# Kernel tuning notes

Hardware: AMD Instinct MI355X
Metric: run time of the kernel (lower is better)

The kernel has to match this reference:

```python
import jax, jax.numpy as jnp
import numpy as np

B, N, H = 2, 4096, 2048
NH, HD = 16, 128
BLK = 256
EPS = 1e-6


def setup_inputs() -> dict:
    key = jax.random.key(0)
    ks = jax.random.split(key, 5)
    scale = 0.02
    x = jax.random.normal(ks[0], (B, N, H), dtype=jnp.float32)
    # ALiBi-style per-head slopes, shape [h,1,1]
    slopes = (1.0 / (2.0 ** (8.0 * np.arange(1, NH + 1) / NH))).astype(np.float32)
    slope_rate = jnp.asarray(slopes).reshape(NH, 1, 1)
    w_qkv = jax.random.normal(ks[1], (3 * NH * HD, H), dtype=jnp.float32) * scale
    w_gate = jax.random.normal(ks[2], (NH * HD, H), dtype=jnp.float32) * scale
    w_out = jax.random.normal(ks[3], (H, NH * HD), dtype=jnp.float32) * scale
    norm_w = jnp.ones((NH * HD,), dtype=jnp.float32)
    return {"hidden_states": x, "slope_rate": slope_rate, "w_qkv": w_qkv,
            "w_gate": w_gate, "w_out": w_out, "norm_w": norm_w}


def _lightning_attn(x, slope_rate, w_qkv, w_gate, w_out, norm_w):
    b, n, _ = x.shape
    h, d = NH, HD
    nb = n // BLK
    # qkv projection + activation
    qkv = jax.nn.silu(jnp.einsum('bnf,of->bno', x, w_qkv))        # [b,n,3hd]
    qkv = qkv.reshape(b, n, h, 3 * d)
    q, k, v = jnp.split(qkv, 3, axis=-1)                          # each [b,n,h,d]
    q = q.transpose(0, 2, 1, 3)                                   # [b,h,n,d]
    k = k.transpose(0, 2, 1, 3)
    v = v.transpose(0, 2, 1, 3)

    s = slope_rate.astype(jnp.float32)                            # [h,1,1]
    arr = jnp.arange(1, BLK + 1, dtype=jnp.float32)               # 1..BLOCK
    q_decay = jnp.exp(-s * arr[:, None])                          # [h,BLK,1]
    k_decay = jnp.exp(-s * (BLK - arr)[:, None])                  # [h,BLK,1]
    idx = arr[:, None] - arr[None, :]                             # [BLK,BLK]
    diag_decay = jnp.where(idx >= 0, jnp.exp(-s * idx), 0.0)      # [h,BLK,BLK]
    block_decay = jnp.exp(-s * BLK)                               # [h,1,1]

    # split sequence into blocks; scan axis leading
    qb = q.reshape(b, h, nb, BLK, d).transpose(2, 0, 1, 3, 4)     # [nb,b,h,BLK,d]
    kb = k.reshape(b, h, nb, BLK, d).transpose(2, 0, 1, 3, 4)
    vb = v.reshape(b, h, nb, BLK, d).transpose(2, 0, 1, 3, 4)

    def step(kv, blk):
        qi, ki, vi = blk                                          # [b,h,BLK,d]
        o_inter = jnp.einsum('bhmd,bhde->bhme', qi * q_decay, kv)
        qk = jnp.einsum('bhmd,bhnd->bhmn', qi, ki) * diag_decay
        o_intra = jnp.einsum('bhmn,bhne->bhme', qk, vi)
        kv_new = block_decay * kv + jnp.einsum('bhmd,bhme->bhde', ki * k_decay, vi)
        return kv_new, o_inter + o_intra

    kv0 = jnp.zeros((b, h, d, d), dtype=jnp.float32)
    _, out = jax.lax.scan(step, kv0, (qb, kb, vb))                # [nb,b,h,BLK,d]
    out = out.transpose(1, 2, 0, 3, 4).reshape(b, h, n, d)        # [b,h,n,d]
    out = out.transpose(0, 2, 1, 3).reshape(b, n, h * d)          # [b,n,h*d]

    # RMSNorm (fp32)
    var = jnp.mean(out * out, axis=-1, keepdims=True)
    out = norm_w * (out * jax.lax.rsqrt(var + EPS))

    gate = jax.nn.sigmoid(jnp.einsum('bnf,of->bno', x, w_gate))
    return jnp.einsum('bno,fo->bnf', gate * out, w_out)


def reference(hidden_states, slope_rate, w_qkv, w_gate, w_out, norm_w):
    return _lightning_attn(hidden_states, slope_rate, w_qkv, w_gate, w_out, norm_w)
```

## Files before the change

kernel.cpp:

```cpp
#include <hip/hip_runtime.h>
#include <hip/hip_bf16.h>
#include <stdint.h>


typedef __bf16 bf16_t;
typedef __bf16 bf16x8 __attribute__((ext_vector_type(8)));
typedef __bf16 bf16x4 __attribute__((ext_vector_type(4)));
typedef float  f32x4  __attribute__((ext_vector_type(4)));

#define AS1C(p) ((const __attribute__((address_space(1))) void*)(p))
#define AS3(p)  ((__attribute__((address_space(3))) void*)(p))

__global__ __launch_bounds__(256) void cvt_kernel(const float* __restrict__ s,
                                                  bf16_t* __restrict__ d, int n4) {
    int i = blockIdx.x * blockDim.x + threadIdx.x;
    const int stride = gridDim.x * blockDim.x;
    for (; i < n4; i += stride) {
        float4 v = ((const float4*)s)[i];
        bf16x4 o;
        o[0] = (bf16_t)v.x; o[1] = (bf16_t)v.y; o[2] = (bf16_t)v.z; o[3] = (bf16_t)v.w;
        ((bf16x4*)d)[i] = o;
    }
}

template <int EPI>
__global__ __launch_bounds__(512)
void gemm6(const bf16_t* __restrict__ A, const bf16_t* __restrict__ Bm,
           int M, int N, int K,
           float* __restrict__ outf, bf16_t* __restrict__ outb,
           bf16_t* __restrict__ qb, bf16_t* __restrict__ kb, bf16_t* __restrict__ vb,
           const float* __restrict__ slopes) {
    __shared__ char lds[2][65536];
    const int tid = threadIdx.x, w = tid >> 6, lane = tid & 63;
    const int l15 = lane & 15, lq = lane >> 4;
    const int wr = w >> 2, wc = w & 3;

    const int nwg = gridDim.x;
    const int cpx = nwg >> 3;
    const int id = blockIdx.x;
    const int sw = (id & 7) * cpx + (id >> 3);
    const int gx = N >> 8;
    const int tm = (sw / gx) << 8;
    const int tn = (sw % gx) << 8;
    const int nt = K >> 6;

    auto stageA1 = [&](char* dst, int t1, int j) {
        const bf16_t* base = A + (size_t)tm * K + t1 * 64;
        const int c = tid + j * 512;
        const int r = c >> 3, sl = c & 7;
        __builtin_amdgcn_global_load_lds(
            AS1C(base + (size_t)r * K + ((sl ^ (r & 7)) << 3)),
            AS3(dst + c * 16), 16, 0, 0);
    };
    auto stageB1 = [&](char* dst, int t1, int j) {
        const bf16_t* base = Bm + (size_t)tn * K + t1 * 64;
        const int c = tid + j * 512;
        const int r = c >> 3, sl = c & 7;
        __builtin_amdgcn_global_load_lds(
            AS1C(base + (size_t)r * K + ((sl ^ (r & 7)) << 3)),
            AS3(dst + 32768 + c * 16), 16, 0, 0);
    };

    f32x4 acc[8][4] = {};

    {
        char* d0 = &lds[0][0];
        stageA1(d0, 0, 0); stageA1(d0, 0, 2);
        stageB1(d0, 0, 0); stageB1(d0, 0, 1); stageB1(d0, 0, 2); stageB1(d0, 0, 3);
        stageA1(d0, 0, 1); stageA1(d0, 0, 3);
    }

    for (int t = 0; t < nt; ++t) {
        const char* cur = &lds[t & 1][0];
        char* nxt = &lds[1 - (t & 1)][0];
        const bool pre = (t + 1 < nt);

        asm volatile("s_waitcnt vmcnt(2)" ::: "memory");
        __builtin_amdgcn_s_barrier();
        __builtin_amdgcn_sched_barrier(0);
        bf16x8 bfr[4][2], af[4][2];
#pragma unroll
        for (int n = 0; n < 4; ++n)
#pragma unroll
            for (int kk = 0; kk < 2; ++kk) {
                const int row = wc * 64 + n * 16 + l15;
                bfr[n][kk] = *(const bf16x8*)(cur + 32768 + row * 128 + ((((kk << 2) | lq) ^ (row & 7)) << 4));
            }
#pragma unroll
        for (int m = 0; m < 4; ++m)
#pragma unroll
            for (int kk = 0; kk < 2; ++kk) {
                const int row = wr * 128 + m * 16 + l15;
                af[m][kk] = *(const bf16x8*)(cur + row * 128 + ((((kk << 2) | lq) ^ (row & 7)) << 4));
            }
        if (pre) {
            stageA1(nxt, t + 1, 0); stageA1(nxt, t + 1, 2);
            stageB1(nxt, t + 1, 0); stageB1(nxt, t + 1, 1);
            stageB1(nxt, t + 1, 2); stageB1(nxt, t + 1, 3);
        }
        __builtin_amdgcn_s_setprio(1);
#pragma unroll
        for (int m = 0; m < 4; ++m)
#pragma unroll
            for (int n = 0; n < 4; ++n)
#pragma unroll
                for (int kk = 0; kk < 2; ++kk)
                    acc[m][n] = __builtin_amdgcn_mfma_f32_16x16x32_bf16(af[m][kk], bfr[n][kk], acc[m][n], 0, 0, 0);
        __builtin_amdgcn_s_setprio(0);

        if (pre) asm volatile("s_waitcnt vmcnt(6)" ::: "memory");
        else     asm volatile("s_waitcnt vmcnt(0)" ::: "memory");
        __builtin_amdgcn_s_barrier();
        __builtin_amdgcn_sched_barrier(0);
#pragma unroll
        for (int m = 0; m < 4; ++m)
#pragma unroll
            for (int kk = 0; kk < 2; ++kk) {
                const int row = wr * 128 + 64 + m * 16 + l15;
                af[m][kk] = *(const bf16x8*)(cur + row * 128 + ((((kk << 2) | lq) ^ (row & 7)) << 4));
            }
        if (pre) {
            stageA1(nxt, t + 1, 1); stageA1(nxt, t + 1, 3);
        }
        __builtin_amdgcn_s_setprio(1);
#pragma unroll
        for (int m = 0; m < 4; ++m)
#pragma unroll
            for (int n = 0; n < 4; ++n)
#pragma unroll
                for (int kk = 0; kk < 2; ++kk)
                    acc[4 + m][n] = __builtin_amdgcn_mfma_f32_16x16x32_bf16(af[m][kk], bfr[n][kk], acc[4 + m][n], 0, 0, 0);
        __builtin_amdgcn_s_setprio(0);
    }

#pragma unroll
    for (int m = 0; m < 8; ++m) {
#pragma unroll
        for (int n = 0; n < 4; ++n) {
            const int colb = tn + wc * 64 + n * 16;
            if (EPI == 2) {
#pragma unroll
                for (int r = 0; r < 4; ++r) {
                    const int row = tm + wr * 128 + m * 16 + lq * 4 + r;
                    outf[(size_t)row * N + colb + l15] = acc[m][n][r];
                }
            } else if (EPI == 1) {
#pragma unroll
                for (int r = 0; r < 4; ++r) {
                    const int row = tm + wr * 128 + m * 16 + lq * 4 + r;
                    const float v = acc[m][n][r];
                    outb[(size_t)row * N + colb + l15] = (bf16_t)(1.f / (1.f + __expf(-v)));
                }
            } else {
                const int head = colb / 384;
                const int jj = colb % 384;
#pragma unroll
                for (int r = 0; r < 4; ++r) {
                    const int row = tm + wr * 128 + m * 16 + lq * 4 + r;
                    const int bidx = row >> 12;
                    const int nn = row & 4095;
                    const float v = acc[m][n][r];
                    const float sv = v / (1.f + __expf(-v));
                    const size_t base = ((size_t)(bidx * 16 + head) * 4096 + nn) * 128;
                    if (jj < 128)       qb[base + jj + l15]       = (bf16_t)sv;
                    else if (jj < 256)  kb[base + jj - 128 + l15] = (bf16_t)sv;
                    else                vb[base + jj - 256 + l15] = (bf16_t)sv;
                }
            }
        }
    }
}

__global__ __launch_bounds__(256)
void transpose_128(const bf16_t* __restrict__ src, bf16_t* __restrict__ dst) {
    __shared__ bf16_t t[64][72];
    const int bh = blockIdx.z;
    const int n0 = blockIdx.x * 64, d0 = blockIdx.y * 64;
    const int tid = threadIdx.x;
    const int r = tid >> 2, cg = (tid & 3) * 16;
    const bf16_t* sp = src + ((size_t)bh * 4096 + n0 + r) * 128 + d0 + cg;
    *(bf16x8*)&t[r][cg] = *(const bf16x8*)sp;
    *(bf16x8*)&t[r][cg + 8] = *(const bf16x8*)(sp + 8);
    __syncthreads();
    bf16_t* dp = dst + ((size_t)bh * 128 + d0 + r) * 4096 + n0 + cg;
#pragma unroll
    for (int i = 0; i < 16; ++i) dp[i] = t[cg + i][r];
}

__global__ __launch_bounds__(256)
void pass_ct(const bf16_t* __restrict__ vT, const bf16_t* __restrict__ kT,
             float* __restrict__ CT, const float* __restrict__ slopes) {
    const int idx = blockIdx.x, bh = idx >> 4, j = idx & 15;
    const float s = slopes[bh & 15];
    const int tid = threadIdx.x, w = tid >> 6, lane = tid & 63;
    const int l15 = lane & 15, lq = lane >> 4;
    const int we = (w & 1) * 64, wd = (w >> 1) * 64;
    const bf16_t* va = vT + (size_t)bh * 524288 + j * 256;
    const bf16_t* ka = kT + (size_t)bh * 524288 + j * 256;
    f32x4 acc[4][4] = {};
#pragma unroll
    for (int kk = 0; kk < 8; ++kk) {
        float fdec[8];
#pragma unroll
        for (int t = 0; t < 8; ++t)
            fdec[t] = __expf(-s * (float)(255 - (kk * 32 + lq * 8 + t)));
        bf16x8 af[4], bfv[4];
#pragma unroll
        for (int et = 0; et < 4; ++et)
            af[et] = *(const bf16x8*)(va + (size_t)(we + et * 16 + l15) * 4096 + kk * 32 + lq * 8);
#pragma unroll
        for (int dt = 0; dt < 4; ++dt) {
            bf16x8 raw = *(const bf16x8*)(ka + (size_t)(wd + dt * 16 + l15) * 4096 + kk * 32 + lq * 8);
#pragma unroll
            for (int t = 0; t < 8; ++t) bfv[dt][t] = (bf16_t)((float)raw[t] * fdec[t]);
        }
#pragma unroll
        for (int et = 0; et < 4; ++et)
#pragma unroll
            for (int dt = 0; dt < 4; ++dt)
                acc[et][dt] = __builtin_amdgcn_mfma_f32_16x16x32_bf16(af[et], bfv[dt], acc[et][dt], 0, 0, 0);
    }
    float* out = CT + (size_t)idx * 16384;
#pragma unroll
    for (int et = 0; et < 4; ++et)
#pragma unroll
        for (int dt = 0; dt < 4; ++dt)
#pragma unroll
            for (int r = 0; r < 4; ++r)
                out[(size_t)(we + et * 16 + lq * 4 + r) * 128 + wd + dt * 16 + l15] = acc[et][dt][r];
}

__global__ __launch_bounds__(256)
void scan_kv(const float* __restrict__ CT, bf16_t* __restrict__ states,
             const float* __restrict__ slopes) {
    const int bh = blockIdx.x;
    const float s = slopes[bh & 15];
    const float bd = __expf(-s * 256.f);
    const int tid = threadIdx.x;
    const int e = tid >> 1, d0 = (tid & 1) * 64;
    const size_t off = (size_t)e * 128 + d0;
    float kv[64];
#pragma unroll
    for (int i = 0; i < 64; ++i) kv[i] = 0.f;
    for (int j = 0; j < 16; ++j) {
        const size_t blk = (size_t)(bh * 16 + j) * 16384;
        bf16_t* st = states + blk + off;
#pragma unroll
        for (int i = 0; i < 64; ++i) st[i] = (bf16_t)kv[i];
        const float* c = CT + blk + off;
#pragma unroll
        for (int i = 0; i < 64; ++i) kv[i] = bd * kv[i] + c[i];
    }
}

__global__ __launch_bounds__(512)
void pass_attn(const bf16_t* __restrict__ qb, const bf16_t* __restrict__ kb,
               const bf16_t* __restrict__ vT, const bf16_t* __restrict__ states,
               const float* __restrict__ slopes, float* __restrict__ outattn) {
    __shared__ bf16_t scratch[8][32][48];
    const int idx = blockIdx.x, bh = idx >> 4, j = idx & 15;
    const int b = bh >> 4, h = bh & 15;
    const int tid = threadIdx.x, w = tid >> 6, lane = tid & 63;
    const int l15 = lane & 15, lq = lane >> 4;
    const float s = slopes[h];
    f32x4 o[2][8] = {};
    float rowf[8];
#pragma unroll
    for (int mt = 0; mt < 2; ++mt)
#pragma unroll
        for (int r = 0; r < 4; ++r) rowf[mt * 4 + r] = __expf(-s * (float)(mt * 16 + lq * 4 + r));

    const size_t qrow = (size_t)bh * 4096 + j * 256;
    const bf16_t* qbp = qb + (qrow + w * 32) * 128;
    const bf16_t* kbp = kb + qrow * 128;
    const bf16_t* vtp = vT + (size_t)bh * 524288 + (size_t)j * 256;

    for (int nc = 0; nc <= w; ++nc) {
        f32x4 sacc[2][2] = {};
#pragma unroll
        for (int kq = 0; kq < 4; ++kq) {
            bf16x8 a2[2], b2[2];
#pragma unroll
            for (int mt = 0; mt < 2; ++mt)
                a2[mt] = *(const bf16x8*)(qbp + (size_t)(mt * 16 + l15) * 128 + kq * 32 + lq * 8);
#pragma unroll
            for (int nt = 0; nt < 2; ++nt)
                b2[nt] = *(const bf16x8*)(kbp + (size_t)(nc * 32 + nt * 16 + l15) * 128 + kq * 32 + lq * 8);
#pragma unroll
            for (int mt = 0; mt < 2; ++mt)
#pragma unroll
                for (int nt = 0; nt < 2; ++nt)
                    sacc[mt][nt] = __builtin_amdgcn_mfma_f32_16x16x32_bf16(a2[mt], b2[nt], sacc[mt][nt], 0, 0, 0);
        }
        float colf[2];
#pragma unroll
        for (int nt = 0; nt < 2; ++nt)
            colf[nt] = __expf(s * (float)(nc * 32 + nt * 16 + l15 - w * 32));
#pragma unroll
        for (int mt = 0; mt < 2; ++mt)
#pragma unroll
            for (int nt = 0; nt < 2; ++nt)
#pragma unroll
                for (int r = 0; r < 4; ++r) {
                    const int mloc = mt * 16 + lq * 4 + r;
                    const int nglob = nc * 32 + nt * 16 + l15;
                    const float f = (w * 32 + mloc >= nglob) ? rowf[mt * 4 + r] * colf[nt] : 0.f;
                    scratch[w][mloc][nt * 16 + l15] = (bf16_t)(sacc[mt][nt][r] * f);
                }
        bf16x8 sa[2];
#pragma unroll
        for (int mt = 0; mt < 2; ++mt)
            sa[mt] = *(const bf16x8*)&scratch[w][mt * 16 + l15][lq * 8];
#pragma unroll
        for (int et = 0; et < 8; ++et) {
            bf16x8 bv = *(const bf16x8*)(vtp + (size_t)(et * 16 + l15) * 4096 + nc * 32 + lq * 8);
#pragma unroll
            for (int mt = 0; mt < 2; ++mt)
                o[mt][et] = __builtin_amdgcn_mfma_f32_16x16x32_bf16(sa[mt], bv, o[mt][et], 0, 0, 0);
        }
    }

    float rq[2];
#pragma unroll
    for (int mt = 0; mt < 2; ++mt)
        rq[mt] = __expf(-s * (float)(w * 32 + mt * 16 + l15 + 1));
    const bf16_t* st = states + (size_t)idx * 16384;
#pragma unroll
    for (int kq = 0; kq < 4; ++kq) {
        bf16x8 aq[2];
#pragma unroll
        for (int mt = 0; mt < 2; ++mt) {
            bf16x8 raw = *(const bf16x8*)(qbp + (size_t)(mt * 16 + l15) * 128 + kq * 32 + lq * 8);
#pragma unroll
            for (int t = 0; t < 8; ++t) aq[mt][t] = (bf16_t)((float)raw[t] * rq[mt]);
        }
#pragma unroll
        for (int et = 0; et < 8; ++et) {
            bf16x8 bs = *(const bf16x8*)(st + (size_t)(et * 16 + l15) * 128 + kq * 32 + lq * 8);
#pragma unroll
            for (int mt = 0; mt < 2; ++mt)
                o[mt][et] = __builtin_amdgcn_mfma_f32_16x16x32_bf16(aq[mt], bs, o[mt][et], 0, 0, 0);
        }
    }

    float* op = outattn + ((size_t)b * 4096 + j * 256 + w * 32) * 2048 + h * 128;
#pragma unroll
    for (int mt = 0; mt < 2; ++mt)
#pragma unroll
        for (int et = 0; et < 8; ++et)
#pragma unroll
            for (int r = 0; r < 4; ++r)
                op[(size_t)(mt * 16 + lq * 4 + r) * 2048 + et * 16 + l15] = o[mt][et][r];
}

__global__ __launch_bounds__(256)
void rmsnorm_gate(const float* __restrict__ attn, const bf16_t* __restrict__ gate_s,
                  const float* __restrict__ norm_w, bf16_t* __restrict__ gout) {
    const int row = blockIdx.x, tid = threadIdx.x;
    const float* ap = attn + (size_t)row * 2048 + tid * 8;
    float4 v0 = *(const float4*)(ap);
    float4 v1 = *(const float4*)(ap + 4);
    float av[8] = {v0.x, v0.y, v0.z, v0.w, v1.x, v1.y, v1.z, v1.w};
    float ss = 0.f;
#pragma unroll
    for (int i = 0; i < 8; ++i) ss += av[i] * av[i];
#pragma unroll
    for (int off = 32; off; off >>= 1) ss += __shfl_xor(ss, off);
    __shared__ float red[4];
    if ((tid & 63) == 0) red[tid >> 6] = ss;
    __syncthreads();
    const float rr = rsqrtf((red[0] + red[1] + red[2] + red[3]) * (1.0f / 2048.f) + 1e-6f);
    const bf16x8 g = *(const bf16x8*)(gate_s + (size_t)row * 2048 + tid * 8);
    const float* nw = norm_w + tid * 8;
    bf16x8 res;
#pragma unroll
    for (int i = 0; i < 8; ++i) res[i] = (bf16_t)((float)g[i] * nw[i] * av[i] * rr);
    *(bf16x8*)(gout + (size_t)row * 2048 + tid * 8) = res;
}

extern "C" void kernel_launch(void* const* d_in, const int* in_sizes, int n_in,
                              void* d_out, int out_size, void* d_ws, size_t ws_size,
                              hipStream_t stream) {
    (void)in_sizes; (void)n_in; (void)out_size;
    const float* x      = (const float*)d_in[0];
    const float* slopes = (const float*)d_in[1];
    const float* w_qkv  = (const float*)d_in[2];
    const float* w_gate = (const float*)d_in[3];
    const float* w_out  = (const float*)d_in[4];
    const float* norm_w = (const float*)d_in[5];
    float* out = (float*)d_out;
    char* ws = (char*)d_ws;

    size_t off = 0;
    auto alloc = [&](size_t bytes) { char* p = ws + off; off += (bytes + 255) & ~(size_t)255; return p; };
    bf16_t* xb     = (bf16_t*)alloc(8192ull * 2048 * 2);
    bf16_t* wqkvb  = (bf16_t*)alloc(6144ull * 2048 * 2);
    bf16_t* wgateb = (bf16_t*)alloc(2048ull * 2048 * 2);
    bf16_t* woutb  = (bf16_t*)alloc(2048ull * 2048 * 2);
    bf16_t* qb     = (bf16_t*)alloc(33554432);
    bf16_t* kb     = (bf16_t*)alloc(33554432);
    bf16_t* vb     = (bf16_t*)alloc(33554432);
    bf16_t* vT     = (bf16_t*)alloc(33554432);
    bf16_t* kT     = (bf16_t*)alloc(33554432);
    if (ws_size < off) return;
    float*  CT     = (float*)vb;
    bf16_t* gate_s = kT;
    bf16_t* states = (bf16_t*)wqkvb;
    bf16_t* gout   = qb;

    cvt_kernel<<<2048, 256, 0, stream>>>(x,      xb,     8192 * 2048 / 4);
    cvt_kernel<<<2048, 256, 0, stream>>>(w_qkv,  wqkvb,  6144 * 2048 / 4);
    cvt_kernel<<<1024, 256, 0, stream>>>(w_gate, wgateb, 2048 * 2048 / 4);
    cvt_kernel<<<1024, 256, 0, stream>>>(w_out,  woutb,  2048 * 2048 / 4);
    gemm6<0><<<768, 512, 0, stream>>>(xb, wqkvb, 8192, 6144, 2048,
        nullptr, nullptr, qb, kb, vb, slopes);
    transpose_128<<<dim3(64, 2, 32), 256, 0, stream>>>(vb, vT);
    transpose_128<<<dim3(64, 2, 32), 256, 0, stream>>>(kb, kT);
    pass_ct<<<512, 256, 0, stream>>>(vT, kT, CT, slopes);
    gemm6<1><<<256, 512, 0, stream>>>(xb, wgateb, 8192, 2048, 2048,
        nullptr, gate_s, nullptr, nullptr, nullptr, nullptr);
    scan_kv<<<32, 256, 0, stream>>>(CT, states, slopes);
    pass_attn<<<512, 512, 0, stream>>>(qb, kb, vT, states, slopes, out);
    rmsnorm_gate<<<8192, 256, 0, stream>>>(out, gate_s, norm_w, gout);
    gemm6<2><<<256, 512, 0, stream>>>(gout, woutb, 8192, 2048, 2048,
        out, nullptr, nullptr, nullptr, nullptr, nullptr);
}
```

Baseline: 574.8 us.

## Split GEMM main loop into four phases interleaving LDS reads, prefetch and MFMA

Restructures the bf16 GEMM inner loop from two phases into four smaller phases, each over one k-half and one m-half. Each phase reads a smaller set of A/B fragments from LDS, issues a slice of the next tile's global-to-LDS prefetch, then runs 16 MFMAs. Staging is spread more evenly across phases with adjusted vmcnt waits. The goal is finer overlap of memory traffic and compute and lower register pressure, at the cost of more barriers per iteration.

Result: slower. 591.5 us (+2.9%).

```diff
diff --git a/kernel.cpp b/kernel.cpp
--- a/kernel.cpp
+++ b/kernel.cpp
@@ -69,68 +69,104 @@
         stageB1(d0, 0, 0); stageB1(d0, 0, 1); stageB1(d0, 0, 2); stageB1(d0, 0, 3);
         stageA1(d0, 0, 1); stageA1(d0, 0, 3);
     }
+    asm volatile("s_waitcnt vmcnt(2)" ::: "memory");
+    __builtin_amdgcn_s_barrier();
+    __builtin_amdgcn_sched_barrier(0);
 
     for (int t = 0; t < nt; ++t) {
         const char* cur = &lds[t & 1][0];
         char* nxt = &lds[1 - (t & 1)][0];
         const bool pre = (t + 1 < nt);
-
-        asm volatile("s_waitcnt vmcnt(2)" ::: "memory");
-        __builtin_amdgcn_s_barrier();
-        __builtin_amdgcn_sched_barrier(0);
-        bf16x8 bfr[4][2], af[4][2];
-#pragma unroll
-        for (int n = 0; n < 4; ++n)
-#pragma unroll
-            for (int kk = 0; kk < 2; ++kk) {
-                const int row = wc * 64 + n * 16 + l15;
-                bfr[n][kk] = *(const bf16x8*)(cur + 32768 + row * 128 + ((((kk << 2) | lq) ^ (row & 7)) << 4));
-            }
+        bf16x8 bfr[4][2], af[4];
+
+#pragma unroll
+        for (int n = 0; n < 4; ++n) {
+            const int row = wc * 64 + n * 16 + l15;
+            bfr[n][0] = *(const bf16x8*)(cur + 32768 + row * 128 + ((lq ^ (row & 7)) << 4));
+        }
+#pragma unroll
+        for (int m = 0; m < 4; ++m) {
+            const int row = wr * 128 + m * 16 + l15;
+            af[m] = *(const bf16x8*)(cur + row * 128 + ((lq ^ (row & 7)) << 4));
+        }
+        if (pre) { stageA1(nxt, t + 1, 0); stageA1(nxt, t + 1, 2); }
+        __builtin_amdgcn_s_barrier();
+        asm volatile("s_waitcnt lgkmcnt(0)" ::: "memory");
+        __builtin_amdgcn_sched_barrier(0);
+        __builtin_amdgcn_s_setprio(1);
 #pragma unroll
         for (int m = 0; m < 4; ++m)
 #pragma unroll
-            for (int kk = 0; kk < 2; ++kk) {
-                const int row = wr * 128 + m * 16 + l15;
-                af[m][kk] = *(const bf16x8*)(cur + row * 128 + ((((kk << 2) | lq) ^ (row & 7)) << 4));
-            }
-        if (pre) {
-            stageA1(nxt, t + 1, 0); stageA1(nxt, t + 1, 2);
-            stageB1(nxt, t + 1, 0); stageB1(nxt, t + 1, 1);
-            stageB1(nxt, t + 1, 2); stageB1(nxt, t + 1, 3);
-        }
+            for (int n = 0; n < 4; ++n)
+                acc[m][n] = __builtin_amdgcn_mfma_f32_16x16x32_bf16(af[m], bfr[n][0], acc[m][n], 0, 0, 0);
+        __builtin_amdgcn_s_setprio(0);
+        __builtin_amdgcn_s_barrier();
+        __builtin_amdgcn_sched_barrier(0);
+
+#pragma unroll
+        for (int n = 0; n < 4; ++n) {
+            const int row = wc * 64 + n * 16 + l15;
+            bfr[n][1] = *(const bf16x8*)(cur + 32768 + row * 128 + (((4 | lq) ^ (row & 7)) << 4));
+        }
+#pragma unroll
+        for (int m = 0; m < 4; ++m) {
+            const int row = wr * 128 + m * 16 + l15;
+            af[m] = *(const bf16x8*)(cur + row * 128 + (((4 | lq) ^ (row & 7)) << 4));
+        }
+        if (pre) { stageB1(nxt, t + 1, 0); stageB1(nxt, t + 1, 1); }
+        __builtin_amdgcn_s_barrier();
+        asm volatile("s_waitcnt lgkmcnt(0)" ::: "memory");
+        __builtin_amdgcn_sched_barrier(0);
         __builtin_amdgcn_s_setprio(1);
 #pragma unroll
         for (int m = 0; m < 4; ++m)
 #pragma unroll
             for (int n = 0; n < 4; ++n)
-#pragma unroll
-                for (int kk = 0; kk < 2; ++kk)
-                    acc[m][n] = __builtin_amdgcn_mfma_f32_16x16x32_bf16(af[m][kk], bfr[n][kk], acc[m][n], 0, 0, 0);
+                acc[m][n] = __builtin_amdgcn_mfma_f32_16x16x32_bf16(af[m], bfr[n][1], acc[m][n], 0, 0, 0);
         __builtin_amdgcn_s_setprio(0);
-
-        if (pre) asm volatile("s_waitcnt vmcnt(6)" ::: "memory");
+        if (pre) asm volatile("s_waitcnt vmcnt(4)" ::: "memory");
         else     asm volatile("s_waitcnt vmcnt(0)" ::: "memory");
         __builtin_amdgcn_s_barrier();
         __builtin_amdgcn_sched_barrier(0);
+
+#pragma unroll
+        for (int m = 0; m < 4; ++m) {
+            const int row = wr * 128 + 64 + m * 16 + l15;
+            af[m] = *(const bf16x8*)(cur + row * 128 + ((lq ^ (row & 7)) << 4));
+        }
+        if (pre) { stageB1(nxt, t + 1, 2); stageB1(nxt, t + 1, 3); }
+        __builtin_amdgcn_s_barrier();
+        asm volatile("s_waitcnt lgkmcnt(0)" ::: "memory");
+        __builtin_amdgcn_sched_barrier(0);
+        __builtin_amdgcn_s_setprio(1);
 #pragma unroll
         for (int m = 0; m < 4; ++m)
 #pragma unroll
-            for (int kk = 0; kk < 2; ++kk) {
-                const int row = wr * 128 + 64 + m * 16 + l15;
-                af[m][kk] = *(const bf16x8*)(cur + row * 128 + ((((kk << 2) | lq) ^ (row & 7)) << 4));
-            }
-        if (pre) {
-            stageA1(nxt, t + 1, 1); stageA1(nxt, t + 1, 3);
-        }
+            for (int n = 0; n < 4; ++n)
+                acc[4 + m][n] = __builtin_amdgcn_mfma_f32_16x16x32_bf16(af[m], bfr[n][0], acc[4 + m][n], 0, 0, 0);
+        __builtin_amdgcn_s_setprio(0);
+        __builtin_amdgcn_s_barrier();
+        __builtin_amdgcn_sched_barrier(0);
+
+#pragma unroll
+        for (int m = 0; m < 4; ++m) {
+            const int row = wr * 128 + 64 + m * 16 + l15;
+            af[m] = *(const bf16x8*)(cur + row * 128 + (((4 | lq) ^ (row & 7)) << 4));
+        }
+        if (pre) { stageA1(nxt, t + 1, 1); stageA1(nxt, t + 1, 3); }
+        __builtin_amdgcn_s_barrier();
+        asm volatile("s_waitcnt lgkmcnt(0)" ::: "memory");
+        __builtin_amdgcn_sched_barrier(0);
         __builtin_amdgcn_s_setprio(1);
 #pragma unroll
         for (int m = 0; m < 4; ++m)
 #pragma unroll
             for (int n = 0; n < 4; ++n)
-#pragma unroll
-                for (int kk = 0; kk < 2; ++kk)
-                    acc[4 + m][n] = __builtin_amdgcn_mfma_f32_16x16x32_bf16(af[m][kk], bfr[n][kk], acc[4 + m][n], 0, 0, 0);
+                acc[4 + m][n] = __builtin_amdgcn_mfma_f32_16x16x32_bf16(af[m], bfr[n][1], acc[4 + m][n], 0, 0, 0);
         __builtin_amdgcn_s_setprio(0);
+        if (pre) asm volatile("s_waitcnt vmcnt(2)" ::: "memory");
+        __builtin_amdgcn_s_barrier();
+        __builtin_amdgcn_sched_barrier(0);
     }
 
 #pragma unroll
```

## Parallelize kv scan per element, balance causal attention rows, reorder GEMM prefetch

Applied to the files above, without the earlier changes.

The kv-state scan now runs one thread per state element across 2048 blocks instead of 32 blocks each holding 64 registers per thread, so it uses far more of the GPU and its memory accesses are coalesced. In the intra-block attention, each wave now takes two 16-row groups (w and 15-w) instead of one contiguous 32-row group. This evens out the triangular causal work across the waves. The GEMM loop issues its next-tile global prefetches before the LDS fragment reads to start memory traffic earlier. Using smaller 16-row tiles means more K loads and less reuse per MFMA.

New measurement: 551.4 us. -4.1%, faster.

```diff
diff --git a/kernel.cpp b/kernel.cpp
--- a/kernel.cpp
+++ b/kernel.cpp
@@ -78,26 +78,26 @@
         asm volatile("s_waitcnt vmcnt(2)" ::: "memory");
         __builtin_amdgcn_s_barrier();
         __builtin_amdgcn_sched_barrier(0);
-        bf16x8 bfr[4][2], af[4][2];
-#pragma unroll
-        for (int n = 0; n < 4; ++n)
-#pragma unroll
-            for (int kk = 0; kk < 2; ++kk) {
-                const int row = wc * 64 + n * 16 + l15;
-                bfr[n][kk] = *(const bf16x8*)(cur + 32768 + row * 128 + ((((kk << 2) | lq) ^ (row & 7)) << 4));
-            }
-#pragma unroll
-        for (int m = 0; m < 4; ++m)
-#pragma unroll
-            for (int kk = 0; kk < 2; ++kk) {
-                const int row = wr * 128 + m * 16 + l15;
-                af[m][kk] = *(const bf16x8*)(cur + row * 128 + ((((kk << 2) | lq) ^ (row & 7)) << 4));
-            }
         if (pre) {
             stageA1(nxt, t + 1, 0); stageA1(nxt, t + 1, 2);
             stageB1(nxt, t + 1, 0); stageB1(nxt, t + 1, 1);
             stageB1(nxt, t + 1, 2); stageB1(nxt, t + 1, 3);
         }
+        bf16x8 bfr[4][2], af[4][2];
+#pragma unroll
+        for (int n = 0; n < 4; ++n)
+#pragma unroll
+            for (int kk = 0; kk < 2; ++kk) {
+                const int row = wc * 64 + n * 16 + l15;
+                bfr[n][kk] = *(const bf16x8*)(cur + 32768 + row * 128 + ((((kk << 2) | lq) ^ (row & 7)) << 4));
+            }
+#pragma unroll
+        for (int m = 0; m < 4; ++m)
+#pragma unroll
+            for (int kk = 0; kk < 2; ++kk) {
+                const int row = wr * 128 + m * 16 + l15;
+                af[m][kk] = *(const bf16x8*)(cur + row * 128 + ((((kk << 2) | lq) ^ (row & 7)) << 4));
+            }
         __builtin_amdgcn_s_setprio(1);
 #pragma unroll
         for (int m = 0; m < 4; ++m)
@@ -112,6 +112,9 @@
         else     asm volatile("s_waitcnt vmcnt(0)" ::: "memory");
         __builtin_amdgcn_s_barrier();
         __builtin_amdgcn_sched_barrier(0);
+        if (pre) {
+            stageA1(nxt, t + 1, 1); stageA1(nxt, t + 1, 3);
+        }
 #pragma unroll
         for (int m = 0; m < 4; ++m)
 #pragma unroll
@@ -119,9 +122,6 @@
                 const int row = wr * 128 + 64 + m * 16 + l15;
                 af[m][kk] = *(const bf16x8*)(cur + row * 128 + ((((kk << 2) | lq) ^ (row & 7)) << 4));
             }
-        if (pre) {
-            stageA1(nxt, t + 1, 1); stageA1(nxt, t + 1, 3);
-        }
         __builtin_amdgcn_s_setprio(1);
 #pragma unroll
         for (int m = 0; m < 4; ++m)
@@ -233,23 +233,17 @@
 __global__ __launch_bounds__(256)
 void scan_kv(const float* __restrict__ CT, bf16_t* __restrict__ states,
              const float* __restrict__ slopes) {
-    const int bh = blockIdx.x;
+    const int gid = blockIdx.x * 256 + threadIdx.x;
+    const int bh = gid >> 14, elem = gid & 16383;
     const float s = slopes[bh & 15];
     const float bd = __expf(-s * 256.f);
-    const int tid = threadIdx.x;
-    const int e = tid >> 1, d0 = (tid & 1) * 64;
-    const size_t off = (size_t)e * 128 + d0;
-    float kv[64];
-#pragma unroll
-    for (int i = 0; i < 64; ++i) kv[i] = 0.f;
+    const float* c = CT + (size_t)bh * 16 * 16384 + elem;
+    bf16_t* st = states + (size_t)bh * 16 * 16384 + elem;
+    float kv = 0.f;
+#pragma unroll
     for (int j = 0; j < 16; ++j) {
-        const size_t blk = (size_t)(bh * 16 + j) * 16384;
-        bf16_t* st = states + blk + off;
-#pragma unroll
-        for (int i = 0; i < 64; ++i) st[i] = (bf16_t)kv[i];
-        const float* c = CT + blk + off;
-#pragma unroll
-        for (int i = 0; i < 64; ++i) kv[i] = bd * kv[i] + c[i];
+        st[(size_t)j * 16384] = (bf16_t)kv;
+        kv = bd * kv + c[(size_t)j * 16384];
     }
 }
 
@@ -257,100 +251,89 @@
 void pass_attn(const bf16_t* __restrict__ qb, const bf16_t* __restrict__ kb,
                const bf16_t* __restrict__ vT, const bf16_t* __restrict__ states,
                const float* __restrict__ slopes, float* __restrict__ outattn) {
-    __shared__ bf16_t scratch[8][32][48];
+    __shared__ bf16_t scratch[8][16][40];
     const int idx = blockIdx.x, bh = idx >> 4, j = idx & 15;
     const int b = bh >> 4, h = bh & 15;
     const int tid = threadIdx.x, w = tid >> 6, lane = tid & 63;
     const int l15 = lane & 15, lq = lane >> 4;
     const float s = slopes[h];
     f32x4 o[2][8] = {};
-    float rowf[8];
-#pragma unroll
-    for (int mt = 0; mt < 2; ++mt)
-#pragma unroll
-        for (int r = 0; r < 4; ++r) rowf[mt * 4 + r] = __expf(-s * (float)(mt * 16 + lq * 4 + r));
+    float rowf[4];
+#pragma unroll
+    for (int r = 0; r < 4; ++r) rowf[r] = __expf(-s * (float)(lq * 4 + r));
 
     const size_t qrow = (size_t)bh * 4096 + j * 256;
-    const bf16_t* qbp = qb + (qrow + w * 32) * 128;
+    const bf16_t* qbase = qb + qrow * 128;
     const bf16_t* kbp = kb + qrow * 128;
     const bf16_t* vtp = vT + (size_t)bh * 524288 + (size_t)j * 256;
 
-    for (int nc = 0; nc <= w; ++nc) {
-        f32x4 sacc[2][2] = {};
-#pragma unroll
-        for (int kq = 0; kq < 4; ++kq) {
-            bf16x8 a2[2], b2[2];
-#pragma unroll
-            for (int mt = 0; mt < 2; ++mt)
-                a2[mt] = *(const bf16x8*)(qbp + (size_t)(mt * 16 + l15) * 128 + kq * 32 + lq * 8);
-#pragma unroll
-            for (int nt = 0; nt < 2; ++nt)
-                b2[nt] = *(const bf16x8*)(kbp + (size_t)(nc * 32 + nt * 16 + l15) * 128 + kq * 32 + lq * 8);
-#pragma unroll
-            for (int mt = 0; mt < 2; ++mt)
-#pragma unroll
-                for (int nt = 0; nt < 2; ++nt)
-                    sacc[mt][nt] = __builtin_amdgcn_mfma_f32_16x16x32_bf16(a2[mt], b2[nt], sacc[mt][nt], 0, 0, 0);
-        }
-        float colf[2];
-#pragma unroll
-        for (int nt = 0; nt < 2; ++nt)
-            colf[nt] = __expf(s * (float)(nc * 32 + nt * 16 + l15 - w * 32));
-#pragma unroll
-        for (int mt = 0; mt < 2; ++mt)
-#pragma unroll
-            for (int nt = 0; nt < 2; ++nt)
+#pragma unroll
+    for (int gi = 0; gi < 2; ++gi) {
+        const int gg = gi ? (15 - w) : w;
+        const bf16_t* qg = qbase + (size_t)(gg * 16) * 128;
+        const int ncmax = gg >> 1;
+        for (int nc = 0; nc <= ncmax; ++nc) {
+            f32x4 sacc[2] = {};
+#pragma unroll
+            for (int kq = 0; kq < 4; ++kq) {
+                bf16x8 a = *(const bf16x8*)(qg + (size_t)l15 * 128 + kq * 32 + lq * 8);
+                bf16x8 b0 = *(const bf16x8*)(kbp + (size_t)(nc * 32 + l15) * 128 + kq * 32 + lq * 8);
+                bf16x8 b1 = *(const bf16x8*)(kbp + (size_t)(nc * 32 + 16 + l15) * 128 + kq * 32 + lq * 8);
+                sacc[0] = __builtin_amdgcn_mfma_f32_16x16x32_bf16(a, b0, sacc[0], 0, 0, 0);
+                sacc[1] = __builtin_amdgcn_mfma_f32_16x16x32_bf16(a, b1, sacc[1], 0, 0, 0);
+            }
+#pragma unroll
+            for (int nt = 0; nt < 2; ++nt) {
+                const float colf = __expf(s * (float)(nc * 32 + nt * 16 + l15 - gg * 16));
 #pragma unroll
                 for (int r = 0; r < 4; ++r) {
-                    const int mloc = mt * 16 + lq * 4 + r;
+                    const int mloc = lq * 4 + r;
                     const int nglob = nc * 32 + nt * 16 + l15;
-                    const float f = (w * 32 + mloc >= nglob) ? rowf[mt * 4 + r] * colf[nt] : 0.f;
-                    scratch[w][mloc][nt * 16 + l15] = (bf16_t)(sacc[mt][nt][r] * f);
+                    const float f = (gg * 16 + mloc >= nglob) ? rowf[r] * colf : 0.f;
+                    scratch[w][mloc][nt * 16 + l15] = (bf16_t)(sacc[nt][r] * f);
                 }
-        bf16x8 sa[2];
-#pragma unroll
-        for (int mt = 0; mt < 2; ++mt)
-            sa[mt] = *(const bf16x8*)&scratch[w][mt * 16 + l15][lq * 8];
-#pragma unroll
-        for (int et = 0; et < 8; ++et) {
-            bf16x8 bv = *(const bf16x8*)(vtp + (size_t)(et * 16 + l15) * 4096 + nc * 32 + lq * 8);
-#pragma unroll
-            for (int mt = 0; mt < 2; ++mt)
-                o[mt][et] = __builtin_amdgcn_mfma_f32_16x16x32_bf16(sa[mt], bv, o[mt][et], 0, 0, 0);
+            }
+            bf16x8 sa = *(const bf16x8*)&scratch[w][l15][lq * 8];
+#pragma unroll
+            for (int et = 0; et < 8; ++et) {
+                bf16x8 bv = *(const bf16x8*)(vtp + (size_t)(et * 16 + l15) * 4096 + nc * 32 + lq * 8);
+                o[gi][et] = __builtin_amdgcn_mfma_f32_16x16x32_bf16(sa, bv, o[gi][et], 0, 0, 0);
+            }
         }
     }
 
     float rq[2];
-#pragma unroll
-    for (int mt = 0; mt < 2; ++mt)
-        rq[mt] = __expf(-s * (float)(w * 32 + mt * 16 + l15 + 1));
+    rq[0] = __expf(-s * (float)(w * 16 + l15 + 1));
+    rq[1] = __expf(-s * (float)((15 - w) * 16 + l15 + 1));
     const bf16_t* st = states + (size_t)idx * 16384;
 #pragma unroll
     for (int kq = 0; kq < 4; ++kq) {
         bf16x8 aq[2];
 #pragma unroll
-        for (int mt = 0; mt < 2; ++mt) {
-            bf16x8 raw = *(const bf16x8*)(qbp + (size_t)(mt * 16 + l15) * 128 + kq * 32 + lq * 8);
-#pragma unroll
-            for (int t = 0; t < 8; ++t) aq[mt][t] = (bf16_t)((float)raw[t] * rq[mt]);
+        for (int gi = 0; gi < 2; ++gi) {
+            const int gg = gi ? (15 - w) : w;
+            bf16x8 raw = *(const bf16x8*)(qbase + (size_t)(gg * 16 + l15) * 128 + kq * 32 + lq * 8);
+#pragma unroll
+            for (int t = 0; t < 8; ++t) aq[gi][t] = (bf16_t)((float)raw[t] * rq[gi]);
         }
 #pragma unroll
         for (int et = 0; et < 8; ++et) {
             bf16x8 bs = *(const bf16x8*)(st + (size_t)(et * 16 + l15) * 128 + kq * 32 + lq * 8);
-#pragma unroll
-            for (int mt = 0; mt < 2; ++mt)
-                o[mt][et] = __builtin_amdgcn_mfma_f32_16x16x32_bf16(aq[mt], bs, o[mt][et], 0, 0, 0);
-        }
-    }
-
-    float* op = outattn + ((size_t)b * 4096 + j * 256 + w * 32) * 2048 + h * 128;
-#pragma unroll
-    for (int mt = 0; mt < 2; ++mt)
+            o[0][et] = __builtin_amdgcn_mfma_f32_16x16x32_bf16(aq[0], bs, o[0][et], 0, 0, 0);
+            o[1][et] = __builtin_amdgcn_mfma_f32_16x16x32_bf16(aq[1], bs, o[1][et], 0, 0, 0);
+        }
+    }
+
+    float* opb = outattn + ((size_t)b * 4096 + j * 256) * 2048 + h * 128;
+#pragma unroll
+    for (int gi = 0; gi < 2; ++gi) {
+        const int gg = gi ? (15 - w) : w;
 #pragma unroll
         for (int et = 0; et < 8; ++et)
 #pragma unroll
             for (int r = 0; r < 4; ++r)
-                op[(size_t)(mt * 16 + lq * 4 + r) * 2048 + et * 16 + l15] = o[mt][et][r];
+                opb[(size_t)(gg * 16 + lq * 4 + r) * 2048 + et * 16 + l15] = o[gi][et][r];
+    }
 }
 
 __global__ __launch_bounds__(256)
@@ -419,7 +402,7 @@
     pass_ct<<<512, 256, 0, stream>>>(vT, kT, CT, slopes);
     gemm6<1><<<256, 512, 0, stream>>>(xb, wgateb, 8192, 2048, 2048,
         nullptr, gate_s, nullptr, nullptr, nullptr, nullptr);
-    scan_kv<<<32, 256, 0, stream>>>(CT, states, slopes);
+    scan_kv<<<2048, 256, 0, stream>>>(CT, states, slopes);
     pass_attn<<<512, 512, 0, stream>>>(qb, kb, vT, states, slopes, out);
     rmsnorm_gate<<<8192, 256, 0, stream>>>(out, gate_s, norm_w, gout);
     gemm6<2><<<256, 512, 0, stream>>>(gout, woutb, 8192, 2048, 2048,
```
